# Optimization experiments

Measured on AMD Instinct MI355X. Metric: run time of the kernel, lower is better.

The kernel has to match this reference:

```python
import jax, jax.numpy as jnp
import numpy as np

N_MODES = 256
N_LAYERS = 4


def _fourier_layer(inp, x, fw_l, lw_l):
    # inp: [B, n_modes] layer state; x: [B, 3] coords
    # tf.signal.rfftnd(..., fft_length=[n_modes]) crops/pads the last axis to
    # n_modes, i.e. uses the first n_modes entries of concat([x, inp], -1).
    d = jnp.concatenate([x, inp], axis=-1)[:, :N_MODES]        # [B, n_modes]
    F = jnp.fft.rfft(d, n=N_MODES, axis=-1)                    # [B, n_modes//2+1]
    x_spatial = jnp.fft.irfft(F * fw_l.astype(F.dtype), n=N_MODES, axis=-1)
    x_spatial = x_spatial.astype(jnp.float32)
    z = inp[:, :N_MODES] * lw_l                                # linear residual branch
    return jax.nn.relu(x_spatial + z)


def setup_inputs() -> dict:
    key = jax.random.key(0)
    ks = jax.random.split(key, 6)
    B, P1, P2, P3 = 262144, 64, N_MODES, 1
    mu = jax.random.normal(ks[0], (B, P1), dtype=jnp.float32)
    x = jax.random.normal(ks[1], (B, 3), dtype=jnp.float32)
    W1 = jax.random.normal(ks[2], (P1, P2), dtype=jnp.float32) * (2.0 / P1) ** 0.5
    b1 = jnp.zeros((P2,), dtype=jnp.float32)
    fw = jax.random.normal(ks[3], (N_LAYERS, N_MODES // 2 + 1), dtype=jnp.float32)
    lw = jax.random.normal(ks[4], (N_LAYERS, N_MODES), dtype=jnp.float32) * 0.1
    W2 = jax.random.normal(ks[5], (P2, P3), dtype=jnp.float32) * (1.0 / P2) ** 0.5
    b2 = jnp.zeros((P3,), dtype=jnp.float32)
    return {"mu": mu, "x": x, "W1": W1, "b1": b1, "fw": fw, "lw": lw, "W2": W2, "b2": b2}


def reference(mu, x, W1, b1, fw, lw, W2, b2):
    # encoder (first_network): dense + relu  -> [B, p_2]
    h = jax.nn.relu(mu @ W1 + b1)
    # stack of Fourier layers (small, structurally distinct loop over n_layers)
    for l in range(N_LAYERS):
        h = _fourier_layer(h, x, fw[l], lw[l])
    # decoder (last_network): dense -> [B, p_3]
    return h @ W2 + b2
```

## Files before the change

### kernel.cpp

```cpp
#include <hip/hip_runtime.h>

#define N_B   262144
#define BM    128
#define KAUG  288
#define LDA   264

typedef _Float16 f16x8 __attribute__((ext_vector_type(8)));
typedef _Float16 f16x4 __attribute__((ext_vector_type(4)));
typedef float    f32x4 __attribute__((ext_vector_type(4)));
typedef float    f32x16 __attribute__((ext_vector_type(16)));

__global__ void fno_precompute(const float* __restrict__ W1,
                               const float* __restrict__ fw,
                               const float* __restrict__ lw,
                               _Float16* __restrict__ Mt,
                               _Float16* __restrict__ W1t)
{
    const int t = threadIdx.x;
    const int b = blockIdx.x;
    if (b < 64) {
        const int l  = b >> 4;
        const int ng = b & 15;
        __shared__ float cosTab[256];
        __shared__ float cs[256];
        cosTab[t] = cosf((float)t * (6.28318530717958647692f / 256.0f));
        __syncthreads();
        {
            const float* fwl = fw + l * 129;
            float s = fwl[0];
            #pragma unroll 4
            for (int k = 1; k < 128; ++k)
                s += 2.0f * fwl[k] * cosTab[(k * t) & 255];
            s += fwl[128] * ((t & 1) ? -1.0f : 1.0f);
            cs[t] = s * (1.0f / 256.0f);
        }
        __syncthreads();
        for (int idx = t; idx < 16 * KAUG; idx += 256) {
            const int n = ng * 16 + idx / KAUG;
            const int k = idx % KAUG;
            float v = 0.0f;
            if (k < 253)               v = cs[(n - k - 3) & 255];
            if (k == n)                v += lw[l * 256 + n];
            if (k >= 256 && k < 259)   v = cs[(n - (k - 256)) & 255];
            Mt[((size_t)l * 256 + n) * KAUG + k] = (_Float16)v;
        }
    } else {
        const int base = (b - 64) * 4096;
        #pragma unroll
        for (int i = 0; i < 16; ++i) {
            const int idx = base + t + i * 256;
            const int n = idx >> 6, k = idx & 63;
            W1t[idx] = (_Float16)W1[k * 256 + n];
        }
    }
}

__global__ __launch_bounds__(256, 2)
void fno_main(const float* __restrict__ mu,
              const float* __restrict__ x,
              const float* __restrict__ b1,
              const float* __restrict__ W2,
              const float* __restrict__ b2,
              const _Float16* __restrict__ Mt,
              const _Float16* __restrict__ W1t,
              float* __restrict__ out)
{
    __shared__ __align__(16) _Float16 hA[(BM + 1) * LDA];
    __shared__ float b1s[256];
    __shared__ float W2s[256];
    __shared__ float red[BM];

    const int t    = threadIdx.x;
    const int w    = t >> 6;
    const int lane = t & 63;
    const int i32  = lane & 31;
    const int q2   = lane >> 5;
    const int r0   = blockIdx.x * BM;
    const int hoff = i32 * LDA + 8 * q2;

    {
        const float4* mu4 = (const float4*)mu + (size_t)r0 * 16;
        #pragma unroll
        for (int j = 0; j < 8; ++j) {
            int f = t + 256 * j;
            int row = f >> 4, c4 = f & 15;
            float4 v = mu4[f];
            f16x4 h;
            h[0] = (_Float16)v.x; h[1] = (_Float16)v.y;
            h[2] = (_Float16)v.z; h[3] = (_Float16)v.w;
            *(f16x4*)&hA[row * LDA + c4 * 4] = h;
        }
        if (t < BM) {
            const float* xp = x + (size_t)(r0 + t) * 3;
            f16x8 hx = {(_Float16)xp[0], (_Float16)xp[1], (_Float16)xp[2],
                        (_Float16)0, (_Float16)0, (_Float16)0,
                        (_Float16)0, (_Float16)0};
            *(f16x8*)&hA[t * LDA + 256] = hx;
        }
        if (t < 33) {
            f16x8 z8 = {};
            *(f16x8*)&hA[BM * LDA + 8 * t] = z8;
        }
        b1s[t] = b1[t];
        W2s[t] = W2[t];
    }
    __syncthreads();

    const f32x16 fz = {0.f,0.f,0.f,0.f, 0.f,0.f,0.f,0.f,
                       0.f,0.f,0.f,0.f, 0.f,0.f,0.f,0.f};
    f32x16 acc[2][4];

    #pragma unroll
    for (int ft = 0; ft < 2; ++ft)
        #pragma unroll
        for (int rt = 0; rt < 4; ++rt) acc[ft][rt] = fz;

    {
        const _Float16* W1p = W1t + (64 * w + i32) * 64 + 8 * q2;
        #pragma unroll
        for (int kc = 0; kc < 4; ++kc) {
            f16x8 mfrag[2];
            #pragma unroll
            for (int ft = 0; ft < 2; ++ft)
                mfrag[ft] = *(const f16x8*)(W1p + 32 * ft * 64 + 16 * kc);
            #pragma unroll
            for (int rt = 0; rt < 4; ++rt) {
                f16x8 hfrag = *(const f16x8*)&hA[hoff + 32 * rt * LDA + 16 * kc];
                #pragma unroll
                for (int ft = 0; ft < 2; ++ft)
                    acc[ft][rt] = __builtin_amdgcn_mfma_f32_32x32x16_f16(
                        mfrag[ft], hfrag, acc[ft][rt], 0, 0, 0);
            }
        }
    }
    __syncthreads();
    #pragma unroll
    for (int ft = 0; ft < 2; ++ft)
        #pragma unroll
        for (int rt = 0; rt < 4; ++rt) {
            const int row = 32 * rt + i32;
            #pragma unroll
            for (int rg = 0; rg < 4; ++rg) {
                const int fb = 64 * w + 32 * ft + 4 * q2 + 8 * rg;
                const float4 bias = *(const float4*)&b1s[fb];
                f16x4 hv;
                hv[0] = (_Float16)fmaxf(acc[ft][rt][4 * rg + 0] + bias.x, 0.f);
                hv[1] = (_Float16)fmaxf(acc[ft][rt][4 * rg + 1] + bias.y, 0.f);
                hv[2] = (_Float16)fmaxf(acc[ft][rt][4 * rg + 2] + bias.z, 0.f);
                hv[3] = (_Float16)fmaxf(acc[ft][rt][4 * rg + 3] + bias.w, 0.f);
                *(f16x4*)&hA[row * LDA + fb] = hv;
            }
        }

    #pragma unroll 1
    for (int l = 0; l < 4; ++l) {
        __syncthreads();
        #pragma unroll
        for (int ft = 0; ft < 2; ++ft)
            #pragma unroll
            for (int rt = 0; rt < 4; ++rt) acc[ft][rt] = fz;

        const _Float16* Mlp = Mt + (size_t)l * 256 * KAUG
                                 + (64 * w + i32) * KAUG + 8 * q2;
        #pragma unroll
        for (int kc = 0; kc < 18; ++kc) {
            f16x8 mfrag[2];
            #pragma unroll
            for (int ft = 0; ft < 2; ++ft)
                mfrag[ft] = *(const f16x8*)(Mlp + 32 * ft * KAUG + 16 * kc);
            #pragma unroll
            for (int rt = 0; rt < 4; ++rt) {
                f16x8 hfrag = *(const f16x8*)&hA[hoff + 32 * rt * LDA + 16 * kc];
                #pragma unroll
                for (int ft = 0; ft < 2; ++ft)
                    acc[ft][rt] = __builtin_amdgcn_mfma_f32_32x32x16_f16(
                        mfrag[ft], hfrag, acc[ft][rt], 0, 0, 0);
            }
        }

        __syncthreads();
        #pragma unroll
        for (int ft = 0; ft < 2; ++ft)
            #pragma unroll
            for (int rt = 0; rt < 4; ++rt) {
                const int row = 32 * rt + i32;
                #pragma unroll
                for (int rg = 0; rg < 4; ++rg) {
                    const int fb = 64 * w + 32 * ft + 4 * q2 + 8 * rg;
                    f16x4 hv;
                    hv[0] = (_Float16)fmaxf(acc[ft][rt][4 * rg + 0], 0.f);
                    hv[1] = (_Float16)fmaxf(acc[ft][rt][4 * rg + 1], 0.f);
                    hv[2] = (_Float16)fmaxf(acc[ft][rt][4 * rg + 2], 0.f);
                    hv[3] = (_Float16)fmaxf(acc[ft][rt][4 * rg + 3], 0.f);
                    *(f16x4*)&hA[row * LDA + fb] = hv;
                }
            }
    }

    __syncthreads();
    {
        const int r  = t & 127;
        const int hf = t >> 7;
        const int n0 = hf * 128;
        float s = 0.f;
        #pragma unroll
        for (int j = 0; j < 16; ++j) {
            f16x8 v = *(const f16x8*)&hA[r * LDA + n0 + 8 * j];
            const float* wp = &W2s[n0 + 8 * j];
            s += (float)v[0] * wp[0] + (float)v[1] * wp[1]
               + (float)v[2] * wp[2] + (float)v[3] * wp[3]
               + (float)v[4] * wp[4] + (float)v[5] * wp[5]
               + (float)v[6] * wp[6] + (float)v[7] * wp[7];
        }
        if (hf) red[r] = s;
        __syncthreads();
        if (!hf) out[r0 + r] = s + red[r] + b2[0];
    }
}

extern "C" void kernel_launch(void* const* d_in, const int* in_sizes, int n_in,
                              void* d_out, int out_size, void* d_ws, size_t ws_size,
                              hipStream_t stream) {
    const float* mu = (const float*)d_in[0];
    const float* x  = (const float*)d_in[1];
    const float* W1 = (const float*)d_in[2];
    const float* b1 = (const float*)d_in[3];
    const float* fw = (const float*)d_in[4];
    const float* lw = (const float*)d_in[5];
    const float* W2 = (const float*)d_in[6];
    const float* b2 = (const float*)d_in[7];
    float* out = (float*)d_out;

    _Float16* Mt  = (_Float16*)d_ws;
    _Float16* W1t = Mt + 4 * 256 * KAUG;

    fno_precompute<<<68, 256, 0, stream>>>(W1, fw, lw, Mt, W1t);
    fno_main<<<N_B / BM, 256, 0, stream>>>(mu, x, b1, W2, b2, Mt, W1t, out);
}
```

Before: 248.9 us.

## Build circulant weight fragments from a shared-memory row table instead of global matrix

Replaces the precomputed dense 256x288 per-layer mixing matrix read from global memory with a small circulant coefficient table (8 shifted copies) staged in LDS, from which MFMA A-fragments are read at computed offsets. The x coordinates are packed into columns 253-255 with the displaced h column moved to a spare slot, so the K loop shrinks from 18 to 16 chunks. The lw residual is now applied in the epilogue from the previous h values. This cuts global/L2 weight traffic and MFMA count, but adds LDS usage, extra table reloads per layer, and special-case index handling for column 252.

```diff
diff --git a/kernel.cpp b/kernel.cpp
--- a/kernel.cpp
+++ b/kernel.cpp
@@ -2,8 +2,8 @@
 
 #define N_B   262144
 #define BM    128
-#define KAUG  288
 #define LDA   264
+#define CSTR  520
 
 typedef _Float16 f16x8 __attribute__((ext_vector_type(8)));
 typedef _Float16 f16x4 __attribute__((ext_vector_type(4)));
@@ -12,40 +12,33 @@
 
 __global__ void fno_precompute(const float* __restrict__ W1,
                                const float* __restrict__ fw,
-                               const float* __restrict__ lw,
-                               _Float16* __restrict__ Mt,
+                               _Float16* __restrict__ csrG,
                                _Float16* __restrict__ W1t)
 {
     const int t = threadIdx.x;
     const int b = blockIdx.x;
-    if (b < 64) {
-        const int l  = b >> 4;
-        const int ng = b & 15;
+    if (b < 4) {
+        const int l = b;
         __shared__ float cosTab[256];
         __shared__ float cs[256];
         cosTab[t] = cosf((float)t * (6.28318530717958647692f / 256.0f));
         __syncthreads();
-        {
-            const float* fwl = fw + l * 129;
-            float s = fwl[0];
-            #pragma unroll 4
-            for (int k = 1; k < 128; ++k)
-                s += 2.0f * fwl[k] * cosTab[(k * t) & 255];
-            s += fwl[128] * ((t & 1) ? -1.0f : 1.0f);
-            cs[t] = s * (1.0f / 256.0f);
-        }
-        __syncthreads();
-        for (int idx = t; idx < 16 * KAUG; idx += 256) {
-            const int n = ng * 16 + idx / KAUG;
-            const int k = idx % KAUG;
-            float v = 0.0f;
-            if (k < 253)               v = cs[(n - k - 3) & 255];
-            if (k == n)                v += lw[l * 256 + n];
-            if (k >= 256 && k < 259)   v = cs[(n - (k - 256)) & 255];
-            Mt[((size_t)l * 256 + n) * KAUG + k] = (_Float16)v;
+        const float* fwl = fw + l * 129;
+        float s = fwl[0];
+        #pragma unroll 4
+        for (int k = 1; k < 128; ++k)
+            s += 2.0f * fwl[k] * cosTab[(k * t) & 255];
+        s += fwl[128] * ((t & 1) ? -1.0f : 1.0f);
+        cs[t] = s * (1.0f / 256.0f);
+        __syncthreads();
+        #pragma unroll
+        for (int j = 0; j < 16; ++j) {
+            const int idx = t + 256 * j;
+            const int p = idx >> 9, i = idx & 511;
+            csrG[l * 4096 + idx] = (_Float16)cs[(1024 - i - p) & 255];
         }
     } else {
-        const int base = (b - 64) * 4096;
+        const int base = (b - 4) * 4096;
         #pragma unroll
         for (int i = 0; i < 16; ++i) {
             const int idx = base + t + i * 256;
@@ -59,15 +52,17 @@
 void fno_main(const float* __restrict__ mu,
               const float* __restrict__ x,
               const float* __restrict__ b1,
+              const float* __restrict__ lw,
               const float* __restrict__ W2,
               const float* __restrict__ b2,
-              const _Float16* __restrict__ Mt,
+              const _Float16* __restrict__ csrG,
               const _Float16* __restrict__ W1t,
               float* __restrict__ out)
 {
-    __shared__ __align__(16) _Float16 hA[(BM + 1) * LDA];
+    __shared__ __align__(16) _Float16 hA[BM * LDA];
+    __shared__ __align__(16) _Float16 csr[8 * CSTR];
     __shared__ float b1s[256];
-    __shared__ float W2s[256];
+    __shared__ float W2s[260];
     __shared__ float red[BM];
 
     const int t    = threadIdx.x;
@@ -77,6 +72,11 @@
     const int q2   = lane >> 5;
     const int r0   = blockIdx.x * BM;
     const int hoff = i32 * LDA + 8 * q2;
+
+    const int blf0 = (3 + 8 * q2 - 64 * w - i32) & 255;
+    const int blf1 = (blf0 - 32) & 255;
+    const int a0   = (blf0 & 7) * CSTR + (blf0 & 248);
+    const int a1   = (blf1 & 7) * CSTR + (blf1 & 248);
 
     {
         const float4* mu4 = (const float4*)mu + (size_t)r0 * 16;
@@ -92,17 +92,19 @@
         }
         if (t < BM) {
             const float* xp = x + (size_t)(r0 + t) * 3;
-            f16x8 hx = {(_Float16)xp[0], (_Float16)xp[1], (_Float16)xp[2],
-                        (_Float16)0, (_Float16)0, (_Float16)0,
-                        (_Float16)0, (_Float16)0};
-            *(f16x8*)&hA[t * LDA + 256] = hx;
-        }
-        if (t < 33) {
-            f16x8 z8 = {};
-            *(f16x8*)&hA[BM * LDA + 8 * t] = z8;
+            hA[t * LDA + 253] = (_Float16)xp[0];
+            hA[t * LDA + 254] = (_Float16)xp[1];
+            hA[t * LDA + 255] = (_Float16)xp[2];
+        }
+        #pragma unroll
+        for (int rep = 0; rep < 2; ++rep) {
+            const int g = t + 256 * rep;
+            const int p = g >> 6, i = (g & 63) * 8;
+            *(f16x8*)&csr[p * CSTR + i] = *(const f16x8*)&csrG[p * 512 + i];
         }
         b1s[t] = b1[t];
-        W2s[t] = W2[t];
+        W2s[t] = (t < 253) ? W2[t] : 0.0f;
+        if (t < 4) W2s[256 + t] = W2[252 + t];
     }
     __syncthreads();
 
@@ -119,17 +121,13 @@
         const _Float16* W1p = W1t + (64 * w + i32) * 64 + 8 * q2;
         #pragma unroll
         for (int kc = 0; kc < 4; ++kc) {
-            f16x8 mfrag[2];
-            #pragma unroll
-            for (int ft = 0; ft < 2; ++ft)
-                mfrag[ft] = *(const f16x8*)(W1p + 32 * ft * 64 + 16 * kc);
+            f16x8 m0 = *(const f16x8*)(W1p + 16 * kc);
+            f16x8 m1 = *(const f16x8*)(W1p + 32 * 64 + 16 * kc);
             #pragma unroll
             for (int rt = 0; rt < 4; ++rt) {
                 f16x8 hfrag = *(const f16x8*)&hA[hoff + 32 * rt * LDA + 16 * kc];
-                #pragma unroll
-                for (int ft = 0; ft < 2; ++ft)
-                    acc[ft][rt] = __builtin_amdgcn_mfma_f32_32x32x16_f16(
-                        mfrag[ft], hfrag, acc[ft][rt], 0, 0, 0);
+                acc[0][rt] = __builtin_amdgcn_mfma_f32_32x32x16_f16(m0, hfrag, acc[0][rt], 0, 0, 0);
+                acc[1][rt] = __builtin_amdgcn_mfma_f32_32x32x16_f16(m1, hfrag, acc[1][rt], 0, 0, 0);
             }
         }
     }
@@ -148,7 +146,12 @@
                 hv[1] = (_Float16)fmaxf(acc[ft][rt][4 * rg + 1] + bias.y, 0.f);
                 hv[2] = (_Float16)fmaxf(acc[ft][rt][4 * rg + 2] + bias.z, 0.f);
                 hv[3] = (_Float16)fmaxf(acc[ft][rt][4 * rg + 3] + bias.w, 0.f);
-                *(f16x4*)&hA[row * LDA + fb] = hv;
+                if (fb == 252) {
+                    hA[row * LDA + 252] = hv[0];
+                    *(f16x4*)&hA[row * LDA + 260] = hv;
+                } else {
+                    *(f16x4*)&hA[row * LDA + fb] = hv;
+                }
             }
         }
 
@@ -160,25 +163,30 @@
             #pragma unroll
             for (int rt = 0; rt < 4; ++rt) acc[ft][rt] = fz;
 
-        const _Float16* Mlp = Mt + (size_t)l * 256 * KAUG
-                                 + (64 * w + i32) * KAUG + 8 * q2;
-        #pragma unroll
-        for (int kc = 0; kc < 18; ++kc) {
-            f16x8 mfrag[2];
-            #pragma unroll
-            for (int ft = 0; ft < 2; ++ft)
-                mfrag[ft] = *(const f16x8*)(Mlp + 32 * ft * KAUG + 16 * kc);
+        #pragma unroll
+        for (int kc = 0; kc < 16; ++kc) {
+            f16x8 m0 = *(const f16x8*)&csr[a0 + 16 * kc];
+            f16x8 m1 = *(const f16x8*)&csr[a1 + 16 * kc];
             #pragma unroll
             for (int rt = 0; rt < 4; ++rt) {
                 f16x8 hfrag = *(const f16x8*)&hA[hoff + 32 * rt * LDA + 16 * kc];
-                #pragma unroll
-                for (int ft = 0; ft < 2; ++ft)
-                    acc[ft][rt] = __builtin_amdgcn_mfma_f32_32x32x16_f16(
-                        mfrag[ft], hfrag, acc[ft][rt], 0, 0, 0);
-            }
-        }
-
-        __syncthreads();
+                acc[0][rt] = __builtin_amdgcn_mfma_f32_32x32x16_f16(m0, hfrag, acc[0][rt], 0, 0, 0);
+                acc[1][rt] = __builtin_amdgcn_mfma_f32_32x32x16_f16(m1, hfrag, acc[1][rt], 0, 0, 0);
+            }
+        }
+        __syncthreads();
+
+        if (l < 3) {
+            #pragma unroll
+            for (int rep = 0; rep < 2; ++rep) {
+                const int g = t + 256 * rep;
+                const int p = g >> 6, i = (g & 63) * 8;
+                *(f16x8*)&csr[p * CSTR + i] =
+                    *(const f16x8*)&csrG[(l + 1) * 4096 + p * 512 + i];
+            }
+        }
+
+        const float* lwl = lw + l * 256;
         #pragma unroll
         for (int ft = 0; ft < 2; ++ft)
             #pragma unroll
@@ -187,12 +195,20 @@
                 #pragma unroll
                 for (int rg = 0; rg < 4; ++rg) {
                     const int fb = 64 * w + 32 * ft + 4 * q2 + 8 * rg;
+                    const int za = row * LDA + ((fb == 252) ? 260 : fb);
+                    f16x4 hp = *(const f16x4*)&hA[za];
+                    float4 lw4 = *(const float4*)(lwl + fb);
                     f16x4 hv;
-                    hv[0] = (_Float16)fmaxf(acc[ft][rt][4 * rg + 0], 0.f);
-                    hv[1] = (_Float16)fmaxf(acc[ft][rt][4 * rg + 1], 0.f);
-                    hv[2] = (_Float16)fmaxf(acc[ft][rt][4 * rg + 2], 0.f);
-                    hv[3] = (_Float16)fmaxf(acc[ft][rt][4 * rg + 3], 0.f);
-                    *(f16x4*)&hA[row * LDA + fb] = hv;
+                    hv[0] = (_Float16)fmaxf(acc[ft][rt][4 * rg + 0] + lw4.x * (float)hp[0], 0.f);
+                    hv[1] = (_Float16)fmaxf(acc[ft][rt][4 * rg + 1] + lw4.y * (float)hp[1], 0.f);
+                    hv[2] = (_Float16)fmaxf(acc[ft][rt][4 * rg + 2] + lw4.z * (float)hp[2], 0.f);
+                    hv[3] = (_Float16)fmaxf(acc[ft][rt][4 * rg + 3] + lw4.w * (float)hp[3], 0.f);
+                    if (fb == 252) {
+                        hA[row * LDA + 252] = hv[0];
+                        *(f16x4*)&hA[row * LDA + 260] = hv;
+                    } else {
+                        *(f16x4*)&hA[row * LDA + fb] = hv;
+                    }
                 }
             }
     }
@@ -212,7 +228,12 @@
                + (float)v[4] * wp[4] + (float)v[5] * wp[5]
                + (float)v[6] * wp[6] + (float)v[7] * wp[7];
         }
-        if (hf) red[r] = s;
+        if (hf) {
+            f16x4 st = *(const f16x4*)&hA[r * LDA + 260];
+            s += (float)st[1] * W2s[257] + (float)st[2] * W2s[258]
+               + (float)st[3] * W2s[259];
+            red[r] = s;
+        }
         __syncthreads();
         if (!hf) out[r0 + r] = s + red[r] + b2[0];
     }
@@ -231,9 +252,9 @@
     const float* b2 = (const float*)d_in[7];
     float* out = (float*)d_out;
 
-    _Float16* Mt  = (_Float16*)d_ws;
-    _Float16* W1t = Mt + 4 * 256 * KAUG;
-
-    fno_precompute<<<68, 256, 0, stream>>>(W1, fw, lw, Mt, W1t);
-    fno_main<<<N_B / BM, 256, 0, stream>>>(mu, x, b1, W2, b2, Mt, W1t, out);
+    _Float16* csrG = (_Float16*)d_ws;
+    _Float16* W1t  = csrG + 4 * 8 * 512;
+
+    fno_precompute<<<8, 256, 0, stream>>>(W1, fw, csrG, W1t);
+    fno_main<<<N_B / BM, 256, 0, stream>>>(mu, x, b1, lw, W2, b2, csrG, W1t, out);
 }
```

Measured after the change: 224.9 us. 9.6% less time.
